# Kernel optimization log

Measured on AMD Instinct MI355X. Metric: run time of the kernel, lower is better.

The kernel has to match this reference:

```python
import jax, jax.numpy as jnp
import numpy as np

C = 512        # concept_num
D = 256        # input_dim / embedding_dim
H = 512        # msg_hidden_dim
M = 256        # msg_output_dim
OH = 512       # hidden_dim
T = 2          # edge_type_num
E = C * (C - 1)  # fully-connected graph without self-loops = 261632


def _glorot(key, shape, fan_in):
    return jax.random.normal(key, shape, jnp.float32) / np.sqrt(fan_in).astype(np.float32)


def setup_inputs() -> dict:
    key = jax.random.key(0)
    ks = jax.random.split(key, 12)
    inputs = jax.random.normal(ks[0], (C, D), jnp.float32)
    rel_type = jax.random.uniform(ks[1], (E, T), jnp.float32)
    send_idx = jax.random.randint(ks[2], (E,), 0, C, jnp.int32)
    rec_idx = jax.random.randint(ks[3], (E,), 0, C, jnp.int32)
    # per-edge-type message MLP params, stacked over type dim
    W1 = _glorot(ks[4], (T, 2 * D, H), 2 * D)
    b1 = jnp.zeros((T, H), jnp.float32)
    W2 = _glorot(ks[5], (T, H, M), H)
    b2 = jnp.zeros((T, M), jnp.float32)
    # output MLP params
    Wo1 = _glorot(ks[6], (M, OH), M)
    bo1 = jnp.zeros((OH,), jnp.float32)
    Wo2 = _glorot(ks[7], (OH, OH), OH)
    bo2 = jnp.zeros((OH,), jnp.float32)
    Wo3 = _glorot(ks[8], (OH, D), OH)
    bo3 = jnp.zeros((D,), jnp.float32)
    return {"inputs": inputs, "rel_type": rel_type, "W1": W1, "b1": b1,
            "W2": W2, "b2": b2, "Wo1": Wo1, "bo1": bo1, "Wo2": Wo2,
            "bo2": bo2, "Wo3": Wo3, "bo3": bo3,
            "send_idx": send_idx, "rec_idx": rec_idx}


def reference(inputs, rel_type, W1, b1, W2, b2, Wo1, bo1, Wo2, bo2, Wo3, bo3,
              send_idx, rec_idx):
    # node2edge: one-hot sparse matmul == index gather
    senders = jnp.take(inputs, send_idx, axis=0)      # [E, D]
    receivers = jnp.take(inputs, rec_idx, axis=0)     # [E, D]
    pre_msg = jnp.concatenate([senders, receivers], axis=-1)  # [E, 2D]
    # per-edge-type MLPs, weighted-summed by rel_type (dropout=0 / eval mode)
    all_msgs = jnp.zeros((pre_msg.shape[0], M), jnp.float32)
    for i in range(T):
        msg = jax.nn.relu(pre_msg @ W1[i] + b1[i])    # [E, H]
        msg = jax.nn.relu(msg @ W2[i] + b2[i])        # [E, M]
        all_msgs = all_msgs + msg * rel_type[:, i:i + 1]
    # edge2node: transposed one-hot sparse matmul == scatter-add over receivers
    agg_msgs = jax.ops.segment_sum(all_msgs, rec_idx, num_segments=inputs.shape[0])  # [C, M]
    pred = jax.nn.relu(agg_msgs @ Wo1 + bo1)
    pred = jax.nn.relu(pred @ Wo2 + bo2)
    return pred @ Wo3 + bo3                           # [C, D]
```

## Files before the change

### kernel.cpp

```cpp
#include <hip/hip_runtime.h>

#define C_N   512
#define E_N   261632
#define CAP   768

typedef _Float16 f16;
typedef _Float16 f16x8_t __attribute__((ext_vector_type(8)));
typedef float    f32x16_t __attribute__((ext_vector_type(16)));

__global__ __launch_bounds__(256) void k_prep_all(
    const float* __restrict__ inputs, const float* __restrict__ W1,
    const float* __restrict__ b1, const float* __restrict__ W2,
    const float* __restrict__ Wo1, const float* __restrict__ Wo2, const float* __restrict__ Wo3,
    f16* __restrict__ SA, f16* __restrict__ RB, f16* __restrict__ W2p,
    f16* __restrict__ Wo1p, f16* __restrict__ Wo2p, f16* __restrict__ Wo3p,
    int* __restrict__ cnt, float* __restrict__ agg)
{
  __shared__ f16 wt[2][256][18];
  int bid = blockIdx.x;
  int tid = threadIdx.x;
  if (bid < 64) {
    int lane = tid & 63, w = tid >> 6;
    int hlf = lane >> 5, l31 = lane & 31;
    int br = bid & 7, bc = (bid >> 3) & 1, mi = bid >> 4;
    int t = mi >> 1, half = mi & 1;
    const float* Wsrc = W1 + (size_t)t * 512 * 512 + (size_t)half * 256 * 512;

    f32x16_t acc[2][2];
    #pragma unroll
    for (int rt = 0; rt < 2; rt++)
      #pragma unroll
      for (int ctl = 0; ctl < 2; ctl++)
        #pragma unroll
        for (int r = 0; r < 16; r++) acc[rt][ctl][r] = 0.f;

    #pragma unroll
    for (int i = 0; i < 4; i++) {
      int idx = tid + i * 256;
      int k = idx >> 6, n4 = idx & 63;
      float4 v = *(const float4*)&Wsrc[(size_t)k * 512 + bc * 256 + n4 * 4];
      wt[0][n4 * 4 + 0][k] = (f16)v.x;
      wt[0][n4 * 4 + 1][k] = (f16)v.y;
      wt[0][n4 * 4 + 2][k] = (f16)v.z;
      wt[0][n4 * 4 + 3][k] = (f16)v.w;
    }

    for (int kc = 0; kc < 16; kc++) {
      __syncthreads();
      if (kc + 1 < 16) {
        int b = (kc + 1) & 1;
        #pragma unroll
        for (int i = 0; i < 4; i++) {
          int idx = tid + i * 256;
          int k = idx >> 6, n4 = idx & 63;
          float4 v = *(const float4*)&Wsrc[(size_t)((kc + 1) * 16 + k) * 512 + bc * 256 + n4 * 4];
          wt[b][n4 * 4 + 0][k] = (f16)v.x;
          wt[b][n4 * 4 + 1][k] = (f16)v.y;
          wt[b][n4 * 4 + 2][k] = (f16)v.z;
          wt[b][n4 * 4 + 3][k] = (f16)v.w;
        }
      }
      f16x8_t af[2];
      #pragma unroll
      for (int rt = 0; rt < 2; rt++) {
        const float4* p = (const float4*)&inputs[(size_t)(br * 64 + rt * 32 + l31) * 256 + kc * 16 + hlf * 8];
        float4 u0 = p[0], u1 = p[1];
        af[rt] = (f16x8_t){(f16)u0.x, (f16)u0.y, (f16)u0.z, (f16)u0.w,
                           (f16)u1.x, (f16)u1.y, (f16)u1.z, (f16)u1.w};
      }
      int b = kc & 1;
      #pragma unroll
      for (int ctl = 0; ctl < 2; ctl++) {
        int n = (2 * w + ctl) * 32 + l31;
        f16x8_t bfr = *(const f16x8_t*)&wt[b][n][hlf * 8];
        #pragma unroll
        for (int rt = 0; rt < 2; rt++)
          acc[rt][ctl] = __builtin_amdgcn_mfma_f32_32x32x16_f16(af[rt], bfr, acc[rt][ctl], 0, 0, 0);
      }
    }
    f16* dst = (half == 0) ? SA : RB;
    #pragma unroll
    for (int ctl = 0; ctl < 2; ctl++) {
      int col = bc * 256 + (2 * w + ctl) * 32 + l31;
      float bias = (half == 1) ? b1[t * 512 + col] : 0.f;
      #pragma unroll
      for (int rt = 0; rt < 2; rt++)
        #pragma unroll
        for (int r = 0; r < 16; r++) {
          int row = br * 64 + rt * 32 + (r & 3) + 8 * (r >> 2) + 4 * hlf;
          dst[((size_t)(t * 512 + row)) * 512 + col] = (f16)(acc[rt][ctl][r] + bias);
        }
    }
  } else if (bid < 192) {
    int gid  = (bid - 64) * 256 + tid;
    int lane = gid & 63;
    int ct   = (gid >> 6) & 7;
    int kc   = (gid >> 9) & 31;
    int t    = gid >> 14;
    int n    = ct * 32 + (lane & 31);
    int k0   = kc * 16 + (lane >> 5) * 8;
    const float* src = W2 + (size_t)t * 512 * 256;
    f16x8_t v;
    #pragma unroll
    for (int j = 0; j < 8; j++) v[j] = (f16)src[(size_t)(k0 + j) * 256 + n];
    *(f16x8_t*)(W2p + (size_t)gid * 8) = v;
  } else if (bid < 256) {
    int gid  = (bid - 192) * 256 + tid;
    int lane = gid & 63;
    int ct   = (gid >> 6) & 15;
    int kc   = gid >> 10;
    int n    = ct * 32 + (lane & 31);
    int k0   = kc * 16 + (lane >> 5) * 8;
    f16x8_t v;
    #pragma unroll
    for (int j = 0; j < 8; j++) v[j] = (f16)Wo1[(size_t)(k0 + j) * 512 + n];
    *(f16x8_t*)(Wo1p + (size_t)gid * 8) = v;
  } else if (bid < 384) {
    int gid  = (bid - 256) * 256 + tid;
    int lane = gid & 63;
    int ct   = (gid >> 6) & 15;
    int kc   = gid >> 10;
    int n    = ct * 32 + (lane & 31);
    int k0   = kc * 16 + (lane >> 5) * 8;
    f16x8_t v;
    #pragma unroll
    for (int j = 0; j < 8; j++) v[j] = (f16)Wo2[(size_t)(k0 + j) * 512 + n];
    *(f16x8_t*)(Wo2p + (size_t)gid * 8) = v;
  } else if (bid < 448) {
    int gid  = (bid - 384) * 256 + tid;
    int lane = gid & 63;
    int ct   = (gid >> 6) & 7;
    int kc   = gid >> 9;
    int n    = ct * 32 + (lane & 31);
    int k0   = kc * 16 + (lane >> 5) * 8;
    f16x8_t v;
    #pragma unroll
    for (int j = 0; j < 8; j++) v[j] = (f16)Wo3[(size_t)(k0 + j) * 256 + n];
    *(f16x8_t*)(Wo3p + (size_t)gid * 8) = v;
  } else if (bid == 448) {
    for (int i = tid; i < 512 * 16; i += 256) cnt[i] = 0;
  } else {
    float4* a4 = (float4*)agg;
    for (int i = tid; i < 512 * 64; i += 256) a4[i] = make_float4(0.f, 0.f, 0.f, 0.f);
  }
}

__global__ __launch_bounds__(512) void k_scatter_d(const int* __restrict__ rec,
    const int* __restrict__ send, const float* __restrict__ rel,
    int* __restrict__ cnt, uint2* __restrict__ smeta)
{
  __shared__ int lh[512];
  __shared__ int lb[512];
  int b = blockIdx.x;
  int e0 = b * (E_N / 128);
  lh[threadIdx.x] = 0;
  __syncthreads();
  for (int i = threadIdx.x; i < E_N / 128; i += 512)
    atomicAdd(&lh[rec[e0 + i]], 1);
  __syncthreads();
  {
    int c = lh[threadIdx.x];
    lb[threadIdx.x] = c ? atomicAdd(&cnt[threadIdx.x * 16], c) : 0;
    lh[threadIdx.x] = 0;
  }
  __syncthreads();
  for (int i = threadIdx.x; i < E_N / 128; i += 512) {
    int e = e0 + i;
    int r = rec[e];
    int p = r * CAP + lb[r] + atomicAdd(&lh[r], 1);
    f16 r0 = (f16)rel[2 * (size_t)e];
    f16 r1 = (f16)rel[2 * (size_t)e + 1];
    unsigned pk = ((unsigned)__builtin_bit_cast(unsigned short, r1) << 16)
                |  (unsigned)__builtin_bit_cast(unsigned short, r0);
    smeta[p] = make_uint2((unsigned)send[e], pk);
  }
}

#define H1S2 264

__global__ __launch_bounds__(512, 4) void k_edges(
    const f16* __restrict__ SA, const f16* __restrict__ RB,
    const f16* __restrict__ W2p, const float* __restrict__ b2,
    const uint2* __restrict__ smeta, const int* __restrict__ cnt,
    float* __restrict__ agg)
{
  __shared__ f16   h1[128 * H1S2];
  __shared__ f16   rbs[2][512];
  __shared__ float b2s[2][256];
  __shared__ float aggL[256];
  __shared__ float relv[128][2];
  __shared__ int   sends[128];

  int c   = blockIdx.x;
  int ti  = blockIdx.y;
  int n_c = cnt[c * 16];
  if (ti * 128 >= n_c) return;

  int tid  = threadIdx.x;
  int lane = tid & 63;
  int w    = tid >> 6;
  int hlf  = lane >> 5;
  int l31  = lane & 31;
  int q5   = tid & 31;
  int rb0  = tid >> 5;

  if (tid < 128) {
    int t = tid >> 6, qq = tid & 63;
    *(f16x8_t*)&rbs[t][qq * 8] = *(const f16x8_t*)&RB[((size_t)(t * 512 + c)) * 512 + qq * 8];
  }
  if (tid < 256) aggL[tid] = 0.0f;
  { int t = (tid >> 8) & 1, col = tid & 255; b2s[t][col] = b2[t * 256 + col]; }

  int s0 = c * CAP + ti * 128;
  int nv = n_c - ti * 128; if (nv > 128) nv = 128;

  if (tid < 128) {
    if (tid < nv) {
      uint2 m = smeta[s0 + tid];
      sends[tid] = (int)m.x;
      relv[tid][0] = (float)__builtin_bit_cast(f16, (unsigned short)(m.y & 0xffffu));
      relv[tid][1] = (float)__builtin_bit_cast(f16, (unsigned short)(m.y >> 16));
    } else {
      sends[tid] = 0; relv[tid][0] = 0.f; relv[tid][1] = 0.f;
    }
  }
  __syncthreads();

  f16x8_t g[8];
  const f16x8_t* SAc = (const f16x8_t*)SA;
  const f16x8_t* Bp  = (const f16x8_t*)W2p;
  f32x16_t acc[4];

  #pragma unroll
  for (int j = 0; j < 8; j++)
    g[j] = SAc[(size_t)sends[rb0 + 16 * j] * 64 + q5];

  for (int ph = 0; ph < 4; ph++) {
    int t  = ph >> 1;
    int kh = ph & 1;

    {
      f16x8_t rbq = *(const f16x8_t*)&rbs[t][(kh * 32 + q5) * 8];
      #pragma unroll
      for (int j = 0; j < 8; j++) {
        int row = rb0 + 16 * j;
        f16x8_t hv;
        #pragma unroll
        for (int e = 0; e < 8; e++) {
          f16 v = (f16)(g[j][e] + rbq[e]);
          hv[e] = (v > (f16)0.0f) ? v : (f16)0.0f;
        }
        *(f16x8_t*)&h1[row * H1S2 + q5 * 8] = hv;
      }
    }
    __syncthreads();

    if (kh == 0) {
      #pragma unroll
      for (int rt = 0; rt < 4; rt++)
        #pragma unroll
        for (int r = 0; r < 16; r++) acc[rt][r] = 0.f;
    }

    f16x8_t bb[2];
    bb[0] = Bp[(size_t)(((t * 32 + kh * 16 + 0) * 8 + w) * 64 + lane)];
    bb[1] = Bp[(size_t)(((t * 32 + kh * 16 + 1) * 8 + w) * 64 + lane)];

    if (ph < 3) {
      int tn  = (ph + 1) >> 1;
      int khn = (ph + 1) & 1;
      #pragma unroll
      for (int j = 0; j < 8; j++)
        g[j] = SAc[(size_t)(tn * 512 + sends[rb0 + 16 * j]) * 64 + khn * 32 + q5];
    }

    for (int kc = 0; kc < 16; kc++) {
      int pb = kc & 1;
      #pragma unroll
      for (int rt = 0; rt < 4; rt++) {
        f16x8_t af = *(const f16x8_t*)&h1[(rt * 32 + l31) * H1S2 + kc * 16 + hlf * 8];
        acc[rt] = __builtin_amdgcn_mfma_f32_32x32x16_f16(af, bb[pb], acc[rt], 0, 0, 0);
      }
      if (kc + 2 < 16)
        bb[pb] = Bp[(size_t)(((t * 32 + kh * 16 + kc + 2) * 8 + w) * 64 + lane)];
    }

    if (kh == 1) {
      int col = w * 32 + l31;
      float b2c = b2s[t][col];
      float csum = 0.0f;
      #pragma unroll
      for (int rt = 0; rt < 4; rt++)
        #pragma unroll
        for (int r = 0; r < 16; r++) {
          int row = rt * 32 + (r & 3) + 8 * (r >> 2) + 4 * hlf;
          float v = fmaxf(acc[rt][r] + b2c, 0.0f);
          csum += v * relv[row][t];
        }
      csum += __shfl_xor(csum, 32, 64);
      if (hlf == 0) aggL[col] += csum;
    }
    __syncthreads();
  }

  if (tid < 256) atomicAdd(&agg[(size_t)c * 256 + tid], aggL[tid]);
}

#define HOS 520

__global__ __launch_bounds__(512, 1) void k_omlp(const float* __restrict__ agg,
    const f16* __restrict__ Wo1p, const float* __restrict__ bo1,
    const f16* __restrict__ Wo2p, const float* __restrict__ bo2,
    const f16* __restrict__ Wo3p, const float* __restrict__ bo3,
    float* __restrict__ out)
{
  __shared__ f16 hL1[32 * HOS];
  __shared__ f16 hL2[32 * HOS];
  int tid = threadIdx.x, lane = tid & 63, w = tid >> 6;
  int hlf = lane >> 5, l31 = lane & 31;
  int br = blockIdx.x;

  {
    f32x16_t acc[2];
    #pragma unroll
    for (int ctl = 0; ctl < 2; ctl++)
      #pragma unroll
      for (int r = 0; r < 16; r++) acc[ctl][r] = 0.f;
    for (int kc = 0; kc < 16; kc++) {
      const float4* p = (const float4*)&agg[(size_t)(br * 32 + l31) * 256 + kc * 16 + hlf * 8];
      float4 u0 = p[0], u1 = p[1];
      f16x8_t af = (f16x8_t){(f16)u0.x, (f16)u0.y, (f16)u0.z, (f16)u0.w,
                             (f16)u1.x, (f16)u1.y, (f16)u1.z, (f16)u1.w};
      #pragma unroll
      for (int ctl = 0; ctl < 2; ctl++) {
        int ct = 2 * w + ctl;
        f16x8_t bfr = *(const f16x8_t*)&Wo1p[((size_t)(kc * 16 + ct) * 64 + lane) * 8];
        acc[ctl] = __builtin_amdgcn_mfma_f32_32x32x16_f16(af, bfr, acc[ctl], 0, 0, 0);
      }
    }
    #pragma unroll
    for (int ctl = 0; ctl < 2; ctl++) {
      int col = (2 * w + ctl) * 32 + l31;
      float bias = bo1[col];
      #pragma unroll
      for (int r = 0; r < 16; r++) {
        int row = (r & 3) + 8 * (r >> 2) + 4 * hlf;
        hL1[row * HOS + col] = (f16)fmaxf(acc[ctl][r] + bias, 0.f);
      }
    }
  }
  __syncthreads();

  {
    f32x16_t acc[2];
    #pragma unroll
    for (int ctl = 0; ctl < 2; ctl++)
      #pragma unroll
      for (int r = 0; r < 16; r++) acc[ctl][r] = 0.f;
    for (int kc = 0; kc < 32; kc++) {
      f16x8_t af = *(const f16x8_t*)&hL1[l31 * HOS + kc * 16 + hlf * 8];
      #pragma unroll
      for (int ctl = 0; ctl < 2; ctl++) {
        int ct = 2 * w + ctl;
        f16x8_t bfr = *(const f16x8_t*)&Wo2p[((size_t)(kc * 16 + ct) * 64 + lane) * 8];
        acc[ctl] = __builtin_amdgcn_mfma_f32_32x32x16_f16(af, bfr, acc[ctl], 0, 0, 0);
      }
    }
    #pragma unroll
    for (int ctl = 0; ctl < 2; ctl++) {
      int col = (2 * w + ctl) * 32 + l31;
      float bias = bo2[col];
      #pragma unroll
      for (int r = 0; r < 16; r++) {
        int row = (r & 3) + 8 * (r >> 2) + 4 * hlf;
        hL2[row * HOS + col] = (f16)fmaxf(acc[ctl][r] + bias, 0.f);
      }
    }
  }
  __syncthreads();

  {
    f32x16_t acc;
    #pragma unroll
    for (int r = 0; r < 16; r++) acc[r] = 0.f;
    for (int kc = 0; kc < 32; kc++) {
      f16x8_t af  = *(const f16x8_t*)&hL2[l31 * HOS + kc * 16 + hlf * 8];
      f16x8_t bfr = *(const f16x8_t*)&Wo3p[((size_t)(kc * 8 + w) * 64 + lane) * 8];
      acc = __builtin_amdgcn_mfma_f32_32x32x16_f16(af, bfr, acc, 0, 0, 0);
    }
    int col = w * 32 + l31;
    float bias = bo3[col];
    #pragma unroll
    for (int r = 0; r < 16; r++) {
      int row = br * 32 + (r & 3) + 8 * (r >> 2) + 4 * hlf;
      out[(size_t)row * 256 + col] = acc[r] + bias;
    }
  }
}

extern "C" void kernel_launch(void* const* d_in, const int* in_sizes, int n_in,
                              void* d_out, int out_size, void* d_ws, size_t ws_size,
                              hipStream_t stream)
{
  (void)in_sizes; (void)n_in; (void)out_size; (void)ws_size;
  const float* inputs = (const float*)d_in[0];
  const float* rel    = (const float*)d_in[1];
  const float* W1     = (const float*)d_in[2];
  const float* b1     = (const float*)d_in[3];
  const float* W2     = (const float*)d_in[4];
  const float* b2     = (const float*)d_in[5];
  const float* Wo1    = (const float*)d_in[6];
  const float* bo1    = (const float*)d_in[7];
  const float* Wo2    = (const float*)d_in[8];
  const float* bo2    = (const float*)d_in[9];
  const float* Wo3    = (const float*)d_in[10];
  const float* bo3    = (const float*)d_in[11];
  const int* send_idx = (const int*)d_in[12];
  const int* rec_idx  = (const int*)d_in[13];
  float* out = (float*)d_out;

  char* ws = (char*)d_ws;
  f16*    SA    = (f16*)   (ws);
  f16*    RB    = (f16*)   (ws + (1024u << 10));
  f16*    W2p   = (f16*)   (ws + (2048u << 10));
  float*  agg   = (float*) (ws + (2560u << 10));
  int*    cnt   = (int*)   (ws + (3072u << 10));
  f16*    Wo1p  = (f16*)   (ws + (3136u << 10));
  f16*    Wo2p  = (f16*)   (ws + (3392u << 10));
  f16*    Wo3p  = (f16*)   (ws + (3904u << 10));
  uint2*  smeta = (uint2*) (ws + (4160u << 10));

  k_prep_all <<<dim3(450),    dim3(256), 0, stream>>>(inputs, W1, b1, W2, Wo1, Wo2, Wo3,
                                                      SA, RB, W2p, Wo1p, Wo2p, Wo3p, cnt, agg);
  k_scatter_d<<<dim3(128),    dim3(512), 0, stream>>>(rec_idx, send_idx, rel, cnt, smeta);
  k_edges    <<<dim3(512, 5), dim3(512), 0, stream>>>(SA, RB, W2p, b2, smeta, cnt, agg);
  k_omlp     <<<dim3(16),     dim3(512), 0, stream>>>(agg, Wo1p, bo1, Wo2p, bo2, Wo3p, bo3, out);
}
```

Measured before the change: 301.3 us.

## Retile edge MFMA into 2x2 warp tiles and skip padded rows

The second-layer GEMM in k_edges is retiled so each warp computes a 64x64 output block (2 row tiles x 2 column tiles) instead of 128 rows x 32 columns. This halves the per-warp LDS A-fragment reads relative to the MFMA count and lets A and B fragments be reused. Row tiles, gathers and h1 builds beyond the valid edge count (rounded to 32) are skipped, so partially filled blocks do less work. The change also vectorises the ReLU/add with elementwise max, transposes relv so rel weights load as float4, and splits aggL per row group. It adds branching on the valid-row count and more B-fragment registers.

```diff
diff --git a/kernel.cpp b/kernel.cpp
--- a/kernel.cpp
+++ b/kernel.cpp
@@ -187,8 +187,8 @@
   __shared__ f16   h1[128 * H1S2];
   __shared__ f16   rbs[2][512];
   __shared__ float b2s[2][256];
-  __shared__ float aggL[256];
-  __shared__ float relv[128][2];
+  __shared__ float aggL[2][256];
+  __shared__ __align__(16) float relv[2][128];
   __shared__ int   sends[128];
 
   int c   = blockIdx.x;
@@ -203,107 +203,161 @@
   int l31  = lane & 31;
   int q5   = tid & 31;
   int rb0  = tid >> 5;
+  int rg   = w >> 2;
+  int cg   = w & 3;
 
   if (tid < 128) {
     int t = tid >> 6, qq = tid & 63;
     *(f16x8_t*)&rbs[t][qq * 8] = *(const f16x8_t*)&RB[((size_t)(t * 512 + c)) * 512 + qq * 8];
   }
-  if (tid < 256) aggL[tid] = 0.0f;
+  ((float*)aggL)[tid] = 0.f;
   { int t = (tid >> 8) & 1, col = tid & 255; b2s[t][col] = b2[t * 256 + col]; }
 
   int s0 = c * CAP + ti * 128;
   int nv = n_c - ti * 128; if (nv > 128) nv = 128;
+  int nv32 = (nv + 31) & ~31;
 
   if (tid < 128) {
     if (tid < nv) {
       uint2 m = smeta[s0 + tid];
       sends[tid] = (int)m.x;
-      relv[tid][0] = (float)__builtin_bit_cast(f16, (unsigned short)(m.y & 0xffffu));
-      relv[tid][1] = (float)__builtin_bit_cast(f16, (unsigned short)(m.y >> 16));
+      relv[0][tid] = (float)__builtin_bit_cast(f16, (unsigned short)(m.y & 0xffffu));
+      relv[1][tid] = (float)__builtin_bit_cast(f16, (unsigned short)(m.y >> 16));
     } else {
-      sends[tid] = 0; relv[tid][0] = 0.f; relv[tid][1] = 0.f;
-    }
-  }
-  __syncthreads();
-
-  f16x8_t g[8];
+      sends[tid] = 0; relv[0][tid] = 0.f; relv[1][tid] = 0.f;
+    }
+  }
+  __syncthreads();
+
   const f16x8_t* SAc = (const f16x8_t*)SA;
   const f16x8_t* Bp  = (const f16x8_t*)W2p;
-  f32x16_t acc[4];
-
+
+  bool use0 = (rg * 64      < nv32);
+  bool use1 = (rg * 64 + 32 < nv32);
+
+  const f16 fz = (f16)0.f;
+  const f16x8_t z8 = {fz, fz, fz, fz, fz, fz, fz, fz};
+
+  f16x8_t g[4];
   #pragma unroll
-  for (int j = 0; j < 8; j++)
-    g[j] = SAc[(size_t)sends[rb0 + 16 * j] * 64 + q5];
+  for (int j = 0; j < 4; j++)
+    if (16 * j < nv32)
+      g[j] = SAc[(size_t)sends[rb0 + 16 * j] * 64 + q5];
+
+  f32x16_t acc[2][2];
 
   for (int ph = 0; ph < 4; ph++) {
     int t  = ph >> 1;
     int kh = ph & 1;
 
-    {
-      f16x8_t rbq = *(const f16x8_t*)&rbs[t][(kh * 32 + q5) * 8];
-      #pragma unroll
-      for (int j = 0; j < 8; j++) {
-        int row = rb0 + 16 * j;
-        f16x8_t hv;
-        #pragma unroll
-        for (int e = 0; e < 8; e++) {
-          f16 v = (f16)(g[j][e] + rbq[e]);
-          hv[e] = (v > (f16)0.0f) ? v : (f16)0.0f;
-        }
-        *(f16x8_t*)&h1[row * H1S2 + q5 * 8] = hv;
-      }
-    }
+    f16x8_t g2[4];
+    #pragma unroll
+    for (int j = 0; j < 4; j++)
+      if (16 * (j + 4) < nv32)
+        g2[j] = SAc[(size_t)(t * 512 + sends[rb0 + 16 * (j + 4)]) * 64 + kh * 32 + q5];
+
+    f16x8_t rbq = *(const f16x8_t*)&rbs[t][(kh * 32 + q5) * 8];
+    #pragma unroll
+    for (int j = 0; j < 4; j++)
+      if (16 * j < nv32) {
+        f16x8_t sv = g[j] + rbq;
+        sv = __builtin_elementwise_max(sv, z8);
+        *(f16x8_t*)&h1[(rb0 + 16 * j) * H1S2 + q5 * 8] = sv;
+      }
+    #pragma unroll
+    for (int j = 0; j < 4; j++)
+      if (16 * (j + 4) < nv32) {
+        f16x8_t sv = g2[j] + rbq;
+        sv = __builtin_elementwise_max(sv, z8);
+        *(f16x8_t*)&h1[(rb0 + 16 * (j + 4)) * H1S2 + q5 * 8] = sv;
+      }
     __syncthreads();
 
     if (kh == 0) {
       #pragma unroll
-      for (int rt = 0; rt < 4; rt++)
-        #pragma unroll
-        for (int r = 0; r < 16; r++) acc[rt][r] = 0.f;
-    }
-
-    f16x8_t bb[2];
-    bb[0] = Bp[(size_t)(((t * 32 + kh * 16 + 0) * 8 + w) * 64 + lane)];
-    bb[1] = Bp[(size_t)(((t * 32 + kh * 16 + 1) * 8 + w) * 64 + lane)];
+      for (int a = 0; a < 2; a++)
+        #pragma unroll
+        for (int b_ = 0; b_ < 2; b_++)
+          #pragma unroll
+          for (int r = 0; r < 16; r++) acc[a][b_][r] = 0.f;
+    }
+
+    const f16x8_t* Bw = Bp + ((size_t)((t * 32 + kh * 16) * 8 + cg * 2) * 64 + lane);
+
+    f16x8_t bb[2][2];
+    if (use0) {
+      bb[0][0] = Bw[0];    bb[0][1] = Bw[64];
+      bb[1][0] = Bw[512];  bb[1][1] = Bw[512 + 64];
+    }
 
     if (ph < 3) {
       int tn  = (ph + 1) >> 1;
       int khn = (ph + 1) & 1;
       #pragma unroll
-      for (int j = 0; j < 8; j++)
-        g[j] = SAc[(size_t)(tn * 512 + sends[rb0 + 16 * j]) * 64 + khn * 32 + q5];
-    }
-
-    for (int kc = 0; kc < 16; kc++) {
-      int pb = kc & 1;
-      #pragma unroll
-      for (int rt = 0; rt < 4; rt++) {
-        f16x8_t af = *(const f16x8_t*)&h1[(rt * 32 + l31) * H1S2 + kc * 16 + hlf * 8];
-        acc[rt] = __builtin_amdgcn_mfma_f32_32x32x16_f16(af, bb[pb], acc[rt], 0, 0, 0);
-      }
-      if (kc + 2 < 16)
-        bb[pb] = Bp[(size_t)(((t * 32 + kh * 16 + kc + 2) * 8 + w) * 64 + lane)];
+      for (int j = 0; j < 4; j++)
+        if (16 * j < nv32)
+          g[j] = SAc[(size_t)(tn * 512 + sends[rb0 + 16 * j]) * 64 + khn * 32 + q5];
+    }
+
+    int a0 = (rg * 64 + l31) * H1S2 + hlf * 8;
+    if (use1) {
+      #pragma unroll
+      for (int kc = 0; kc < 16; kc++) {
+        int pb = kc & 1;
+        f16x8_t af0 = *(const f16x8_t*)&h1[a0 + kc * 16];
+        f16x8_t af1 = *(const f16x8_t*)&h1[a0 + 32 * H1S2 + kc * 16];
+        acc[0][0] = __builtin_amdgcn_mfma_f32_32x32x16_f16(af0, bb[pb][0], acc[0][0], 0, 0, 0);
+        acc[0][1] = __builtin_amdgcn_mfma_f32_32x32x16_f16(af0, bb[pb][1], acc[0][1], 0, 0, 0);
+        acc[1][0] = __builtin_amdgcn_mfma_f32_32x32x16_f16(af1, bb[pb][0], acc[1][0], 0, 0, 0);
+        acc[1][1] = __builtin_amdgcn_mfma_f32_32x32x16_f16(af1, bb[pb][1], acc[1][1], 0, 0, 0);
+        if (kc + 2 < 16) {
+          bb[pb][0] = Bw[(kc + 2) * 512];
+          bb[pb][1] = Bw[(kc + 2) * 512 + 64];
+        }
+      }
+    } else if (use0) {
+      #pragma unroll
+      for (int kc = 0; kc < 16; kc++) {
+        int pb = kc & 1;
+        f16x8_t af0 = *(const f16x8_t*)&h1[a0 + kc * 16];
+        acc[0][0] = __builtin_amdgcn_mfma_f32_32x32x16_f16(af0, bb[pb][0], acc[0][0], 0, 0, 0);
+        acc[0][1] = __builtin_amdgcn_mfma_f32_32x32x16_f16(af0, bb[pb][1], acc[0][1], 0, 0, 0);
+        if (kc + 2 < 16) {
+          bb[pb][0] = Bw[(kc + 2) * 512];
+          bb[pb][1] = Bw[(kc + 2) * 512 + 64];
+        }
+      }
     }
 
     if (kh == 1) {
-      int col = w * 32 + l31;
-      float b2c = b2s[t][col];
-      float csum = 0.0f;
-      #pragma unroll
-      for (int rt = 0; rt < 4; rt++)
-        #pragma unroll
-        for (int r = 0; r < 16; r++) {
-          int row = rt * 32 + (r & 3) + 8 * (r >> 2) + 4 * hlf;
-          float v = fmaxf(acc[rt][r] + b2c, 0.0f);
-          csum += v * relv[row][t];
+      #pragma unroll
+      for (int ctl = 0; ctl < 2; ctl++) {
+        int col = (cg * 2 + ctl) * 32 + l31;
+        float b2c = b2s[t][col];
+        float csum = 0.f;
+        #pragma unroll
+        for (int rt = 0; rt < 2; rt++) {
+          if (rg * 64 + rt * 32 < nv32) {
+            int rbase = rg * 64 + rt * 32 + 4 * hlf;
+            #pragma unroll
+            for (int grp = 0; grp < 4; grp++) {
+              float4 rv = *(const float4*)&relv[t][rbase + 8 * grp];
+              float v0 = fmaxf(acc[rt][ctl][grp * 4 + 0] + b2c, 0.f);
+              float v1 = fmaxf(acc[rt][ctl][grp * 4 + 1] + b2c, 0.f);
+              float v2 = fmaxf(acc[rt][ctl][grp * 4 + 2] + b2c, 0.f);
+              float v3 = fmaxf(acc[rt][ctl][grp * 4 + 3] + b2c, 0.f);
+              csum += v0 * rv.x + v1 * rv.y + v2 * rv.z + v3 * rv.w;
+            }
+          }
         }
-      csum += __shfl_xor(csum, 32, 64);
-      if (hlf == 0) aggL[col] += csum;
+        csum += __shfl_xor(csum, 32, 64);
+        if (hlf == 0) aggL[rg][col] += csum;
+      }
     }
     __syncthreads();
   }
 
-  if (tid < 256) atomicAdd(&agg[(size_t)c * 256 + tid], aggL[tid]);
+  if (tid < 256) atomicAdd(&agg[(size_t)c * 256 + tid], aggL[0][tid] + aggL[1][tid]);
 }
 
 #define HOS 520
```

New measurement: 339.1 us. 1.13x slower.
